# Optimization experiments

Hardware: AMD Instinct MI355X
Metric: run time of the kernel (lower is better)

The kernel has to match this reference:

```python
import jax, jax.numpy as jnp
import numpy as np

B, T, D, H, DK, DV = 2, 2048, 1024, 16, 64, 64
_MASK_ADDER = -10000.0  # tf-models MaskedSoftmax convention


def setup_inputs() -> dict:
    key = jax.random.key(0)
    ks = jax.random.split(key, 8)
    s = 0.02
    return {
        "query": jax.random.normal(ks[0], (B, T, D), jnp.float32),
        "value": jax.random.normal(ks[1], (B, T, D), jnp.float32),
        "Wq": jax.random.normal(ks[2], (D, H, DK), jnp.float32) * s,
        "bq": jnp.zeros((H, DK), jnp.float32),
        "Wk": jax.random.normal(ks[3], (D, H, DK), jnp.float32) * s,
        "bk": jnp.zeros((H, DK), jnp.float32),
        "Wv": jax.random.normal(ks[4], (D, H, DV), jnp.float32) * s,
        "bv": jnp.zeros((H, DV), jnp.float32),
        "Wo": jax.random.normal(ks[5], (H, DV, D), jnp.float32) * s,
        "bo": jnp.zeros((D,), jnp.float32),
        "attention_mask": jnp.ones((B, T, T), jnp.int32),
    }


def reference(query, value, Wq, bq, Wk, bk, Wv, bv, Wo, bo, attention_mask):
    # key defaults to value (call() with key=None); training=False -> no dropout
    q = jnp.einsum("btd,dhk->bthk", query, Wq) + bq          # [B,T,H,DK]
    k = jnp.einsum("bsd,dhk->bshk", value, Wk) + bk          # [B,S,H,DK]
    v = jnp.einsum("bsd,dhk->bshk", value, Wv) + bv          # [B,S,H,DV]
    q = q * (1.0 / jnp.sqrt(jnp.asarray(DK, q.dtype)))
    scores = jnp.einsum("bthk,bshk->bhts", q, k)             # [B,H,T,S]
    # MaskedSoftmax: expand mask at axis 1, additive -10000 on masked slots
    adder = (1.0 - attention_mask.astype(scores.dtype))[:, None, :, :] * _MASK_ADDER
    probs = jax.nn.softmax(scores + adder, axis=-1)
    ctx = jnp.einsum("bhts,bshv->bthv", probs, v)            # [B,T,H,DV]
    out = jnp.einsum("bthv,hvd->btd", ctx, Wo) + bo          # [B,T,D]
    return out
```

## Files before the change

kernel.cpp:

```cpp
#include <hip/hip_runtime.h>
#include <hip/hip_bf16.h>
#include <stdint.h>

#define TSEQ 2048
#define DMODEL 1024
#define NHEAD 16
#define HDIM 64
#define MROWS 4096
#define L2E 1.44269504088896340736f

typedef unsigned short u16;
typedef unsigned int u32;
typedef __attribute__((ext_vector_type(8))) short bf16x8;
typedef __attribute__((ext_vector_type(8))) unsigned short u16x8;
typedef __attribute__((ext_vector_type(4))) unsigned short u16x4;
typedef __attribute__((ext_vector_type(4))) float f32x4;
typedef __attribute__((ext_vector_type(16))) float f32x16;
typedef __attribute__((ext_vector_type(4))) unsigned int u32x4;

__device__ inline u16 f2bf(float f) {
  __hip_bfloat16 h(f);
  return __builtin_bit_cast(u16, h);
}

__device__ inline float fexp2(float x) { float r; asm("v_exp_f32 %0, %1" : "=v"(r) : "v"(x)); return r; }

__device__ inline unsigned cvtpk_bf16(float a, float b) {
  unsigned r; asm("v_cvt_pk_bf16_f32 %0, %1, %2" : "=v"(r) : "v"(a), "v"(b)); return r;
}

__device__ inline void permswap(u32& a, u32& b) {
  asm volatile("v_permlane32_swap_b32 %0, %1" : "+v"(a), "+v"(b));
}

__device__ inline void gload16(const void* g, void* l) {
  __builtin_amdgcn_global_load_lds((const __attribute__((address_space(1))) void*)g,
                                   (__attribute__((address_space(3))) void*)l, 16, 0, 0);
}

__global__ void cvt2(const float* __restrict__ q, const float* __restrict__ v,
                     u16* __restrict__ qo, u16* __restrict__ vo) {
  const float* in = blockIdx.y ? v : q;
  u16* out = blockIdx.y ? vo : qo;
  int i = (blockIdx.x * blockDim.x + threadIdx.x) * 4;
  float4 x = *(const float4*)(in + i);
  u16x4 o;
  o.x = f2bf(x.x); o.y = f2bf(x.y); o.z = f2bf(x.z); o.w = f2bf(x.w);
  *(u16x4*)(out + i) = o;
}

__global__ void wtrans4(const float* __restrict__ Wq, const float* __restrict__ Wk,
                        const float* __restrict__ Wv, const float* __restrict__ Wo,
                        u16* __restrict__ WT3, u16* __restrict__ WoT) {
  __shared__ float tile[32][33];
  const int z = blockIdx.z;
  const float* W = z == 0 ? Wq : z == 1 ? Wk : z == 2 ? Wv : Wo;
  u16* WT = z < 3 ? (WT3 + (size_t)z * 1024 * 1024) : WoT;
  const int bx = blockIdx.x, by = blockIdx.y;
  const int tr = threadIdx.x >> 3;
  const int tc4 = (threadIdx.x & 7) * 4;
  float4 v = *(const float4*)(W + (size_t)(by * 32 + tr) * 1024 + bx * 32 + tc4);
  tile[tr][tc4 + 0] = v.x; tile[tr][tc4 + 1] = v.y;
  tile[tr][tc4 + 2] = v.z; tile[tr][tc4 + 3] = v.w;
  __syncthreads();
  u16x4 o;
  o.x = f2bf(tile[tc4 + 0][tr]); o.y = f2bf(tile[tc4 + 1][tr]);
  o.z = f2bf(tile[tc4 + 2][tr]); o.w = f2bf(tile[tc4 + 3][tr]);
  *(u16x4*)(WT + (size_t)(bx * 32 + tr) * 1024 + by * 32 + tc4) = o;
}

__global__ void maskflag(const int* __restrict__ mask, int* __restrict__ flags) {
  const int st = blockIdx.x, qt = blockIdx.y, b = blockIdx.z;
  const int row = qt * 128 + (threadIdx.x >> 1);
  const int col0 = st * 128 + (threadIdx.x & 1) * 64;
  const int* p = mask + (size_t)b * TSEQ * TSEQ + (size_t)row * TSEQ + col0;
  int ok = 1;
  #pragma unroll
  for (int j = 0; j < 64; j += 4) {
    int4 v = *(const int4*)(p + j);
    ok &= (v.x == 1) & (v.y == 1) & (v.z == 1) & (v.w == 1);
  }
  ok = __all(ok);
  __shared__ int s[4];
  if ((threadIdx.x & 63) == 0) s[threadIdx.x >> 6] = ok;
  __syncthreads();
  if (threadIdx.x == 0) flags[(b * 16 + qt) * 16 + st] = s[0] & s[1] & s[2] & s[3];
}

__global__ void vtrans(const u16* __restrict__ V, u16* __restrict__ VT) {
  __shared__ u16 tile[64][72];
  const int bh = blockIdx.y;
  const int t0 = blockIdx.x * 64;
  const u16* src = V + ((size_t)bh * TSEQ + t0) * 64;
  const int r = threadIdx.x >> 3, sg = threadIdx.x & 7;
  #pragma unroll
  for (int i = 0; i < 2; ++i) {
    int row = r + i * 32;
    u16x8 v = *(const u16x8*)(src + (size_t)row * 64 + sg * 8);
    #pragma unroll
    for (int j = 0; j < 8; ++j) tile[row][sg * 8 + j] = v[j];
  }
  __syncthreads();
  u16* dst = VT + (size_t)bh * 64 * TSEQ;
  #pragma unroll
  for (int i = 0; i < 2; ++i) {
    int v = r + i * 32;
    u16x8 o;
    #pragma unroll
    for (int j = 0; j < 8; ++j) o[j] = tile[sg * 8 + j][v];
    *(u16x8*)(dst + (size_t)v * TSEQ + t0 + sg * 8) = o;
  }
}

__global__ __launch_bounds__(256) void gemm_qkv(
    const u16* __restrict__ qxb, const u16* __restrict__ vxb, const u16* __restrict__ WT3,
    const float* __restrict__ bq, const float* __restrict__ bk, const float* __restrict__ bv,
    u16* __restrict__ Qb, u16* __restrict__ Kb, u16* __restrict__ Vb, float qscale) {
  __shared__ u16 As[128 * 64];
  __shared__ u16 Bs[128 * 64];
  const int tid = threadIdx.x;
  const int w = tid >> 6, lane = tid & 63;
  const int lo = lane & 15, hi = lane >> 4;
  const int m0 = blockIdx.x * 128, n0 = blockIdx.y * 128;
  const int nsel = n0 >> 10;
  const u16* A = nsel == 0 ? qxb : vxb;
  const float* bias = nsel == 0 ? bq : nsel == 1 ? bk : bv;
  u16* dst = nsel == 0 ? Qb : nsel == 1 ? Kb : Vb;
  const float scl = nsel == 0 ? qscale : 1.0f;
  const int wm = (w >> 1) * 64, wn = (w & 1) * 64;
  f32x4 acc[4][4] = {};
  const int loff = w * 4096 + lane * 16;
  for (int kt = 0; kt < 16; ++kt) {
    #pragma unroll
    for (int i = 0; i < 4; ++i) {
      const int off = loff + i * 1024;
      const int row = off >> 7;
      const int g = ((off >> 4) & 7) ^ (row & 7);
      gload16(A + (size_t)(m0 + row) * 1024 + kt * 64 + g * 8, (char*)As + off);
      gload16(WT3 + (size_t)(n0 + row) * 1024 + kt * 64 + g * 8, (char*)Bs + off);
    }
    __syncthreads();
    #pragma unroll
    for (int kk = 0; kk < 2; ++kk) {
      bf16x8 af[4], bfr[4];
      #pragma unroll
      for (int mi = 0; mi < 4; ++mi) {
        int row = wm + mi * 16 + lo;
        af[mi] = *(const bf16x8*)(As + row * 64 + (((kk * 4 + hi) ^ (row & 7)) << 3));
      }
      #pragma unroll
      for (int ni = 0; ni < 4; ++ni) {
        int row = wn + ni * 16 + lo;
        bfr[ni] = *(const bf16x8*)(Bs + row * 64 + (((kk * 4 + hi) ^ (row & 7)) << 3));
      }
      #pragma unroll
      for (int mi = 0; mi < 4; ++mi)
        #pragma unroll
        for (int ni = 0; ni < 4; ++ni)
          acc[mi][ni] = __builtin_amdgcn_mfma_f32_16x16x32_bf16(af[mi], bfr[ni], acc[mi][ni], 0, 0, 0);
    }
    __syncthreads();
  }
  #pragma unroll
  for (int ni = 0; ni < 4; ++ni) {
    const int col = (n0 + wn + ni * 16 + lo) & 1023;
    const float bc = bias[col];
    #pragma unroll
    for (int mi = 0; mi < 4; ++mi) {
      #pragma unroll
      for (int r = 0; r < 4; ++r) {
        const int row = m0 + wm + mi * 16 + hi * 4 + r;
        const float v = (acc[mi][ni][r] + bc) * scl;
        dst[(size_t)(((row >> 11) * NHEAD + (col >> 6)) * TSEQ + (row & 2047)) * HDIM + (col & 63)] = f2bf(v);
      }
    }
  }
}

__global__ __launch_bounds__(256) void gemm_o(const u16* __restrict__ A, const u16* __restrict__ BT,
                                              const float* __restrict__ bias, float* __restrict__ C) {
  __shared__ u16 As[64 * 64];
  __shared__ u16 Bs[128 * 64];
  const int tid = threadIdx.x;
  const int w = tid >> 6, lane = tid & 63;
  const int lo = lane & 15, hi = lane >> 4;
  const int m0 = blockIdx.x * 64, n0 = blockIdx.y * 128;
  const int wm = (w >> 1) * 32, wn = (w & 1) * 64;
  f32x4 acc[2][4] = {};
  for (int kt = 0; kt < 16; ++kt) {
    #pragma unroll
    for (int i = 0; i < 2; ++i) {
      const int off = tid * 16 + i * 4096;
      const int row = off >> 7;
      const int g = ((off >> 4) & 7) ^ (row & 7);
      gload16(A + (size_t)(m0 + row) * 1024 + kt * 64 + g * 8, (char*)As + off);
    }
    #pragma unroll
    for (int i = 0; i < 4; ++i) {
      const int off = tid * 16 + i * 4096;
      const int row = off >> 7;
      const int g = ((off >> 4) & 7) ^ (row & 7);
      gload16(BT + (size_t)(n0 + row) * 1024 + kt * 64 + g * 8, (char*)Bs + off);
    }
    __syncthreads();
    #pragma unroll
    for (int kk = 0; kk < 2; ++kk) {
      bf16x8 af[2], bfr[4];
      #pragma unroll
      for (int mi = 0; mi < 2; ++mi) {
        int row = wm + mi * 16 + lo;
        af[mi] = *(const bf16x8*)(As + row * 64 + (((kk * 4 + hi) ^ (row & 7)) << 3));
      }
      #pragma unroll
      for (int ni = 0; ni < 4; ++ni) {
        int row = wn + ni * 16 + lo;
        bfr[ni] = *(const bf16x8*)(Bs + row * 64 + (((kk * 4 + hi) ^ (row & 7)) << 3));
      }
      #pragma unroll
      for (int mi = 0; mi < 2; ++mi)
        #pragma unroll
        for (int ni = 0; ni < 4; ++ni)
          acc[mi][ni] = __builtin_amdgcn_mfma_f32_16x16x32_bf16(af[mi], bfr[ni], acc[mi][ni], 0, 0, 0);
    }
    __syncthreads();
  }
  #pragma unroll
  for (int ni = 0; ni < 4; ++ni) {
    const int col = n0 + wn + ni * 16 + lo;
    const float bc = bias[col];
    #pragma unroll
    for (int mi = 0; mi < 2; ++mi)
      #pragma unroll
      for (int r = 0; r < 4; ++r) {
        const int row = m0 + wm + mi * 16 + hi * 4 + r;
        C[(size_t)row * DMODEL + col] = acc[mi][ni][r] + bc;
      }
  }
}

__global__ __launch_bounds__(256) void flash(
    const u16* __restrict__ Q, const u16* __restrict__ K, const u16* __restrict__ VT,
    const int* __restrict__ mask, const int* __restrict__ flags, u16* __restrict__ ctx) {
  __shared__ u16 Ks[2][64 * 64];
  __shared__ u16 Vs[3][64 * 64];
  const int tid = threadIdx.x, w = tid >> 6, lane = tid & 63;
  const int l5 = lane & 31, hi2 = lane >> 5;
  const int qt = blockIdx.x, bh = blockIdx.y;
  const int b = bh >> 4, h = bh & 15;
  const int tq = qt * 128 + w * 32;

  const int soff = w * 2048 + lane * 16;
  const int srow0 = w * 16 + (lane >> 3);
  const int lg0 = (((lane & 7) ^ (lane >> 3) ^ ((w * 2) & 3)) << 3);
  const int lg1 = (((lane & 7) ^ (lane >> 3) ^ ((w * 2 + 1) & 3)) << 3);

  bf16x8 qf[4];
  #pragma unroll
  for (int kc = 0; kc < 4; ++kc)
    qf[kc] = *(const bf16x8*)(Q + ((size_t)bh * TSEQ + tq + l5) * 64 + kc * 16 + hi2 * 8);

  unsigned fl = 0;
  {
    const int* fp = flags + (b * 16 + qt) * 16;
    #pragma unroll
    for (int i = 0; i < 4; ++i) {
      int4 v = *(const int4*)(fp + i * 4);
      fl |= (unsigned)((v.x & 1) | ((v.y & 1) << 1) | ((v.z & 1) << 2) | ((v.w & 1) << 3)) << (4 * i);
    }
  }

  f32x16 o0 = {}, o1 = {};
  float mrow = -1e30f, lrow = 0.f;
  bf16x8 paA[4], paB[4];

#define STAGE_K(buf, st_) do {                                                        \
    const u16* kb_ = K + ((size_t)bh * TSEQ + (st_) * 64) * 64;                       \
    gload16(kb_ + (size_t)srow0 * 64 + lg0, (char*)Ks[buf] + soff);                   \
    gload16(kb_ + (size_t)(srow0 + 8) * 64 + lg1, (char*)Ks[buf] + soff + 1024);      \
  } while (0)
#define STAGE_V(buf, st_) do {                                                        \
    const u16* vb_ = VT + (size_t)bh * 64 * TSEQ + (st_) * 64;                        \
    gload16(vb_ + (size_t)srow0 * TSEQ + lg0, (char*)Vs[buf] + soff);                 \
    gload16(vb_ + (size_t)(srow0 + 8) * TSEQ + lg1, (char*)Vs[buf] + soff + 1024);    \
  } while (0)

#define FR(base, row, sg) \
  (*(const bf16x8*)((base) + (row) * 64 + ((((sg) ^ ((row) & 7) ^ (((row) >> 3) & 3)) << 3))))

#define QKC(T, S0, S1) do {                                                           \
    const u16* Kb_ = Ks[(T) & 1];                                                     \
    _Pragma("unroll") for (int kc = 0; kc < 4; ++kc) {                                \
      const int sg = kc * 2 + hi2;                                                    \
      S0 = __builtin_amdgcn_mfma_f32_32x32x16_bf16(FR(Kb_, l5, sg), qf[kc], S0, 0, 0, 0); \
      S1 = __builtin_amdgcn_mfma_f32_32x32x16_bf16(FR(Kb_, 32 + l5, sg), qf[kc], S1, 0, 0, 0); \
    } } while (0)

#define PVC(VB, PA) do {                                                              \
    const u16* Vb_ = Vs[VB];                                                          \
    _Pragma("unroll") for (int kc = 0; kc < 4; ++kc) {                                \
      const int sg = kc * 2 + hi2;                                                    \
      o0 = __builtin_amdgcn_mfma_f32_32x32x16_bf16(PA[kc], FR(Vb_, l5, sg), o0, 0, 0, 0); \
      o1 = __builtin_amdgcn_mfma_f32_32x32x16_bf16(PA[kc], FR(Vb_, 32 + l5, sg), o1, 0, 0, 0); \
    } } while (0)

#define SMAX(T, S0, S1, PAOUT) do {                                                   \
    if (!((fl >> ((T) >> 1)) & 1)) {                                                  \
      const int t_ = tq + l5;                                                         \
      const int* mp_ = mask + ((size_t)b * TSEQ + t_) * TSEQ + (T) * 64;              \
      _Pragma("unroll") for (int r = 0; r < 16; ++r) {                                \
        const int sr_ = (r & 3) + 8 * (r >> 2) + 4 * hi2;                             \
        S0[r] += (1.0f - (float)mp_[sr_]) * -14426.950408f;                           \
        S1[r] += (1.0f - (float)mp_[sr_ + 32]) * -14426.950408f;                      \
      } }                                                                             \
    float c0 = fmaxf(S0[0], S1[0]), c1 = fmaxf(S0[1], S1[1]);                         \
    float c2 = fmaxf(S0[2], S1[2]), c3 = fmaxf(S0[3], S1[3]);                         \
    _Pragma("unroll") for (int r = 4; r < 16; r += 4) {                               \
      c0 = fmaxf(c0, fmaxf(S0[r], S1[r]));     c1 = fmaxf(c1, fmaxf(S0[r+1], S1[r+1])); \
      c2 = fmaxf(c2, fmaxf(S0[r+2], S1[r+2])); c3 = fmaxf(c3, fmaxf(S0[r+3], S1[r+3])); } \
    float pm = fmaxf(fmaxf(c0, c1), fmaxf(c2, c3));                                   \
    pm = fmaxf(pm, __shfl_xor(pm, 32));                                               \
    if (__any(pm - mrow > 11.0f)) {                                                   \
      const float mn_ = fmaxf(mrow, pm);                                              \
      const float a_ = fexp2(mrow - mn_);                                             \
      lrow *= a_; mrow = mn_;                                                         \
      _Pragma("unroll") for (int r = 0; r < 16; ++r) {                                \
        const float ar_ = __shfl(a_, (r & 3) + 8 * (r >> 2) + 4 * hi2);               \
        o0[r] *= ar_; o1[r] *= ar_; } }                                               \
    float rs = 0.f; u32 W0_[8], W1_[8];                                               \
    _Pragma("unroll") for (int q_ = 0; q_ < 4; ++q_)                                  \
      _Pragma("unroll") for (int c_ = 0; c_ < 2; ++c_) {                              \
        const int r = 4 * q_ + 2 * c_;                                                \
        float a0 = fexp2(S0[r] - mrow), b0 = fexp2(S0[r + 1] - mrow);                 \
        float a1 = fexp2(S1[r] - mrow), b1 = fexp2(S1[r + 1] - mrow);                 \
        rs += (a0 + b0) + (a1 + b1);                                                  \
        W0_[q_ * 2 + c_] = cvtpk_bf16(a0, b0);                                        \
        W1_[q_ * 2 + c_] = cvtpk_bf16(a1, b1); }                                      \
    rs += __shfl_xor(rs, 32); lrow += rs;                                             \
    _Pragma("unroll") for (int ts = 0; ts < 2; ++ts)                                  \
      _Pragma("unroll") for (int qp = 0; qp < 2; ++qp) {                              \
        u32 d0 = ts ? W1_[(2 * qp) * 2 + 0] : W0_[(2 * qp) * 2 + 0];                  \
        u32 e0 = ts ? W1_[(2 * qp + 1) * 2 + 0] : W0_[(2 * qp + 1) * 2 + 0];          \
        u32 d1 = ts ? W1_[(2 * qp) * 2 + 1] : W0_[(2 * qp) * 2 + 1];                  \
        u32 e1 = ts ? W1_[(2 * qp + 1) * 2 + 1] : W0_[(2 * qp + 1) * 2 + 1];          \
        permswap(d0, e0); permswap(d1, e1);                                           \
        u32x4 fw_; fw_.x = d0; fw_.y = d1; fw_.z = e0; fw_.w = e1;                    \
        PAOUT[ts * 2 + qp] = __builtin_bit_cast(bf16x8, fw_); }                       \
  } while (0)

#define BODY(T, VPREV, VNEXT, DOSTAGE, PAIN, PAOUT) do {                              \
    if (DOSTAGE) { STAGE_K(((T) + 1) & 1, (T) + 1); STAGE_V(VNEXT, (T) + 1); }        \
    f32x16 s0 = {}, s1 = {};                                                          \
    __builtin_amdgcn_s_setprio(1);                                                    \
    QKC(T, s0, s1);                                                                   \
    PVC(VPREV, PAIN);                                                                 \
    __builtin_amdgcn_s_setprio(0);                                                    \
    SMAX(T, s0, s1, PAOUT);                                                           \
    __syncthreads();                                                                  \
  } while (0)

  STAGE_K(0, 0); STAGE_V(0, 0);
  __syncthreads();
  {
    f32x16 s0 = {}, s1 = {};
    __builtin_amdgcn_s_setprio(1);
    QKC(0, s0, s1);
    __builtin_amdgcn_s_setprio(0);
    STAGE_K(1, 1); STAGE_V(1, 1);
    SMAX(0, s0, s1, paA);
    __syncthreads();
  }

  int vp = 0, vn = 2;
  for (int t = 1; t < 31; t += 2) {
    BODY(t, vp, vn, 1, paA, paB);
    const int vp2 = (vp + 1 == 3) ? 0 : vp + 1;
    const int vn2 = (vn + 1 == 3) ? 0 : vn + 1;
    BODY(t + 1, vp2, vn2, 1, paB, paA);
    vp = (vp2 + 1 == 3) ? 0 : vp2 + 1;
    vn = (vn2 + 1 == 3) ? 0 : vn2 + 1;
  }
  BODY(31, vp, 0, 0, paA, paB);

  __builtin_amdgcn_s_setprio(1);
  PVC(1, paB);
  __builtin_amdgcn_s_setprio(0);

#undef BODY
#undef SMAX
#undef PVC
#undef QKC
#undef FR
#undef STAGE_V
#undef STAGE_K

  const float inv = 1.0f / lrow;
  #pragma unroll
  for (int r = 0; r < 16; ++r) {
    const int sr = (r & 3) + 8 * (r >> 2) + 4 * hi2;
    const float ir = __shfl(inv, sr);
    u16* cp = ctx + (size_t)(b * TSEQ + tq + sr) * DMODEL + h * 64;
    cp[l5] = f2bf(o0[r] * ir);
    cp[32 + l5] = f2bf(o1[r] * ir);
  }
}

extern "C" void kernel_launch(void* const* d_in, const int* in_sizes, int n_in,
                              void* d_out, int out_size, void* d_ws, size_t ws_size,
                              hipStream_t stream) {
  (void)in_sizes; (void)n_in; (void)out_size; (void)ws_size;
  const float* query = (const float*)d_in[0];
  const float* value = (const float*)d_in[1];
  const float* Wq = (const float*)d_in[2];
  const float* bq = (const float*)d_in[3];
  const float* Wk = (const float*)d_in[4];
  const float* bk = (const float*)d_in[5];
  const float* Wv = (const float*)d_in[6];
  const float* bv = (const float*)d_in[7];
  const float* Wo = (const float*)d_in[8];
  const float* bo = (const float*)d_in[9];
  const int* amask = (const int*)d_in[10];

  char* ws = (char*)d_ws;
  const size_t MB = 1 << 20;
  u16* qxb = (u16*)(ws + 0 * MB);
  u16* vxb = (u16*)(ws + 8 * MB);
  u16* WT3 = (u16*)(ws + 16 * MB);
  u16* WoT = (u16*)(ws + 22 * MB);
  u16* Qb  = (u16*)(ws + 24 * MB);
  u16* Kb  = (u16*)(ws + 32 * MB);
  u16* Vb  = (u16*)(ws + 40 * MB);
  u16* VTb = (u16*)(ws + 48 * MB);
  u16* ctx = (u16*)(ws + 56 * MB);
  int* flg = (int*)(ws + 64 * MB);

  cvt2<<<dim3(4096, 2), 256, 0, stream>>>(query, value, qxb, vxb);
  wtrans4<<<dim3(32, 32, 4), 256, 0, stream>>>(Wq, Wk, Wv, Wo, WT3, WoT);
  maskflag<<<dim3(16, 16, 2), 256, 0, stream>>>(amask, flg);

  gemm_qkv<<<dim3(32, 24), 256, 0, stream>>>(qxb, vxb, WT3, bq, bk, bv, Qb, Kb, Vb, 0.125f * L2E);
  vtrans<<<dim3(32, 32), 256, 0, stream>>>(Vb, VTb);
  flash<<<dim3(16, 32), 256, 0, stream>>>(Qb, Kb, VTb, amask, flg, ctx);
  gemm_o<<<dim3(64, 8), 256, 0, stream>>>(ctx, WoT, bo, (float*)d_out);
}
```

Measured before the change: 144.7 us.

## Merge prep kernels, write V transposed from QKV GEMM, swizzle block order

Combines the fp32-to-bf16 conversion, weight transpose and mask-flag kernels into one launch. The QKV GEMM epilogue now writes V directly in transposed layout, which removes the separate vtrans kernel and its round trip through memory. Block indices in gemm_qkv, gemm_o and flash are remapped into XCD-style groups to improve cache locality. The softmax row max uses v_max3. Together these cut launch overhead and extra traffic, at the cost of strided 8-byte stores in the V epilogue.

```diff
diff --git a/kernel.cpp b/kernel.cpp
--- a/kernel.cpp
+++ b/kernel.cpp
@@ -29,6 +29,10 @@
   unsigned r; asm("v_cvt_pk_bf16_f32 %0, %1, %2" : "=v"(r) : "v"(a), "v"(b)); return r;
 }
 
+__device__ inline float fmax3(float a, float b, float c) {
+  float r; asm("v_max3_f32 %0, %1, %2, %3" : "=v"(r) : "v"(a), "v"(b), "v"(c)); return r;
+}
+
 __device__ inline void permswap(u32& a, u32& b) {
   asm volatile("v_permlane32_swap_b32 %0, %1" : "+v"(a), "+v"(b));
 }
@@ -38,94 +42,73 @@
                                    (__attribute__((address_space(3))) void*)l, 16, 0, 0);
 }
 
-__global__ void cvt2(const float* __restrict__ q, const float* __restrict__ v,
-                     u16* __restrict__ qo, u16* __restrict__ vo) {
-  const float* in = blockIdx.y ? v : q;
-  u16* out = blockIdx.y ? vo : qo;
-  int i = (blockIdx.x * blockDim.x + threadIdx.x) * 4;
-  float4 x = *(const float4*)(in + i);
-  u16x4 o;
-  o.x = f2bf(x.x); o.y = f2bf(x.y); o.z = f2bf(x.z); o.w = f2bf(x.w);
-  *(u16x4*)(out + i) = o;
-}
-
-__global__ void wtrans4(const float* __restrict__ Wq, const float* __restrict__ Wk,
-                        const float* __restrict__ Wv, const float* __restrict__ Wo,
-                        u16* __restrict__ WT3, u16* __restrict__ WoT) {
+__global__ void prep(const float* __restrict__ q, const float* __restrict__ v,
+                     u16* __restrict__ qo, u16* __restrict__ vo,
+                     const float* __restrict__ Wq, const float* __restrict__ Wk,
+                     const float* __restrict__ Wv, const float* __restrict__ Wo,
+                     u16* __restrict__ WT3, u16* __restrict__ WoT,
+                     const int* __restrict__ mask, int* __restrict__ flags) {
   __shared__ float tile[32][33];
-  const int z = blockIdx.z;
-  const float* W = z == 0 ? Wq : z == 1 ? Wk : z == 2 ? Wv : Wo;
-  u16* WT = z < 3 ? (WT3 + (size_t)z * 1024 * 1024) : WoT;
-  const int bx = blockIdx.x, by = blockIdx.y;
-  const int tr = threadIdx.x >> 3;
-  const int tc4 = (threadIdx.x & 7) * 4;
-  float4 v = *(const float4*)(W + (size_t)(by * 32 + tr) * 1024 + bx * 32 + tc4);
-  tile[tr][tc4 + 0] = v.x; tile[tr][tc4 + 1] = v.y;
-  tile[tr][tc4 + 2] = v.z; tile[tr][tc4 + 3] = v.w;
-  __syncthreads();
-  u16x4 o;
-  o.x = f2bf(tile[tc4 + 0][tr]); o.y = f2bf(tile[tc4 + 1][tr]);
-  o.z = f2bf(tile[tc4 + 2][tr]); o.w = f2bf(tile[tc4 + 3][tr]);
-  *(u16x4*)(WT + (size_t)(bx * 32 + tr) * 1024 + by * 32 + tc4) = o;
-}
-
-__global__ void maskflag(const int* __restrict__ mask, int* __restrict__ flags) {
-  const int st = blockIdx.x, qt = blockIdx.y, b = blockIdx.z;
-  const int row = qt * 128 + (threadIdx.x >> 1);
-  const int col0 = st * 128 + (threadIdx.x & 1) * 64;
-  const int* p = mask + (size_t)b * TSEQ * TSEQ + (size_t)row * TSEQ + col0;
-  int ok = 1;
-  #pragma unroll
-  for (int j = 0; j < 64; j += 4) {
-    int4 v = *(const int4*)(p + j);
-    ok &= (v.x == 1) & (v.y == 1) & (v.z == 1) & (v.w == 1);
-  }
-  ok = __all(ok);
-  __shared__ int s[4];
-  if ((threadIdx.x & 63) == 0) s[threadIdx.x >> 6] = ok;
-  __syncthreads();
-  if (threadIdx.x == 0) flags[(b * 16 + qt) * 16 + st] = s[0] & s[1] & s[2] & s[3];
-}
-
-__global__ void vtrans(const u16* __restrict__ V, u16* __restrict__ VT) {
-  __shared__ u16 tile[64][72];
-  const int bh = blockIdx.y;
-  const int t0 = blockIdx.x * 64;
-  const u16* src = V + ((size_t)bh * TSEQ + t0) * 64;
-  const int r = threadIdx.x >> 3, sg = threadIdx.x & 7;
-  #pragma unroll
-  for (int i = 0; i < 2; ++i) {
-    int row = r + i * 32;
-    u16x8 v = *(const u16x8*)(src + (size_t)row * 64 + sg * 8);
-    #pragma unroll
-    for (int j = 0; j < 8; ++j) tile[row][sg * 8 + j] = v[j];
-  }
-  __syncthreads();
-  u16* dst = VT + (size_t)bh * 64 * TSEQ;
-  #pragma unroll
-  for (int i = 0; i < 2; ++i) {
-    int v = r + i * 32;
-    u16x8 o;
-    #pragma unroll
-    for (int j = 0; j < 8; ++j) o[j] = tile[sg * 8 + j][v];
-    *(u16x8*)(dst + (size_t)v * TSEQ + t0 + sg * 8) = o;
+  __shared__ int sred[4];
+  const int bid = blockIdx.x, tid = threadIdx.x;
+  if (bid < 8192) {
+    const float* in = bid < 4096 ? q : v;
+    u16* out = bid < 4096 ? qo : vo;
+    const int i = (bid & 4095) * 1024 + tid * 4;
+    float4 x = *(const float4*)(in + i);
+    u16x4 o;
+    o.x = f2bf(x.x); o.y = f2bf(x.y); o.z = f2bf(x.z); o.w = f2bf(x.w);
+    *(u16x4*)(out + i) = o;
+  } else if (bid < 12288) {
+    int t = bid - 8192;
+    const int z = t >> 10; t &= 1023;
+    const float* W = z == 0 ? Wq : z == 1 ? Wk : z == 2 ? Wv : Wo;
+    u16* WT = z < 3 ? (WT3 + (size_t)z * 1024 * 1024) : WoT;
+    const int bx = t & 31, by = t >> 5;
+    const int tr = tid >> 3;
+    const int tc4 = (tid & 7) * 4;
+    float4 x = *(const float4*)(W + (size_t)(by * 32 + tr) * 1024 + bx * 32 + tc4);
+    tile[tr][tc4 + 0] = x.x; tile[tr][tc4 + 1] = x.y;
+    tile[tr][tc4 + 2] = x.z; tile[tr][tc4 + 3] = x.w;
+    __syncthreads();
+    u16x4 o;
+    o.x = f2bf(tile[tc4 + 0][tr]); o.y = f2bf(tile[tc4 + 1][tr]);
+    o.z = f2bf(tile[tc4 + 2][tr]); o.w = f2bf(tile[tc4 + 3][tr]);
+    *(u16x4*)(WT + (size_t)(bx * 32 + tr) * 1024 + by * 32 + tc4) = o;
+  } else {
+    const int t = bid - 12288;
+    const int st = t & 15, qt = (t >> 4) & 15, b = t >> 8;
+    const int row = qt * 128 + (tid >> 1);
+    const int col0 = st * 128 + (tid & 1) * 64;
+    const int* p = mask + (size_t)b * TSEQ * TSEQ + (size_t)row * TSEQ + col0;
+    int ok = 1;
+    #pragma unroll
+    for (int j = 0; j < 64; j += 4) {
+      int4 x = *(const int4*)(p + j);
+      ok &= (x.x == 1) & (x.y == 1) & (x.z == 1) & (x.w == 1);
+    }
+    ok = __all(ok);
+    if ((tid & 63) == 0) sred[tid >> 6] = ok;
+    __syncthreads();
+    if (tid == 0) flags[(b * 16 + qt) * 16 + st] = sred[0] & sred[1] & sred[2] & sred[3];
   }
 }
 
 __global__ __launch_bounds__(256) void gemm_qkv(
     const u16* __restrict__ qxb, const u16* __restrict__ vxb, const u16* __restrict__ WT3,
     const float* __restrict__ bq, const float* __restrict__ bk, const float* __restrict__ bv,
-    u16* __restrict__ Qb, u16* __restrict__ Kb, u16* __restrict__ Vb, float qscale) {
+    u16* __restrict__ Qb, u16* __restrict__ Kb, u16* __restrict__ VTb, float qscale) {
   __shared__ u16 As[128 * 64];
   __shared__ u16 Bs[128 * 64];
   const int tid = threadIdx.x;
   const int w = tid >> 6, lane = tid & 63;
   const int lo = lane & 15, hi = lane >> 4;
-  const int m0 = blockIdx.x * 128, n0 = blockIdx.y * 128;
+  const int bid = blockIdx.x + (blockIdx.y << 5);
+  const int swz = (bid & 7) * 96 + (bid >> 3);
+  const int m0 = (swz & 31) << 7, n0 = (swz >> 5) << 7;
   const int nsel = n0 >> 10;
   const u16* A = nsel == 0 ? qxb : vxb;
   const float* bias = nsel == 0 ? bq : nsel == 1 ? bk : bv;
-  u16* dst = nsel == 0 ? Qb : nsel == 1 ? Kb : Vb;
   const float scl = nsel == 0 ? qscale : 1.0f;
   const int wm = (w >> 1) * 64, wn = (w & 1) * 64;
   f32x4 acc[4][4] = {};
@@ -161,17 +144,36 @@
     }
     __syncthreads();
   }
-  #pragma unroll
-  for (int ni = 0; ni < 4; ++ni) {
-    const int col = (n0 + wn + ni * 16 + lo) & 1023;
-    const float bc = bias[col];
-    #pragma unroll
-    for (int mi = 0; mi < 4; ++mi) {
-      #pragma unroll
-      for (int r = 0; r < 4; ++r) {
-        const int row = m0 + wm + mi * 16 + hi * 4 + r;
-        const float v = (acc[mi][ni][r] + bc) * scl;
-        dst[(size_t)(((row >> 11) * NHEAD + (col >> 6)) * TSEQ + (row & 2047)) * HDIM + (col & 63)] = f2bf(v);
+  if (nsel < 2) {
+    u16* dst = nsel == 0 ? Qb : Kb;
+    #pragma unroll
+    for (int ni = 0; ni < 4; ++ni) {
+      const int col = (n0 + wn + ni * 16 + lo) & 1023;
+      const float bc = bias[col];
+      #pragma unroll
+      for (int mi = 0; mi < 4; ++mi) {
+        #pragma unroll
+        for (int r = 0; r < 4; ++r) {
+          const int row = m0 + wm + mi * 16 + hi * 4 + r;
+          const float v = (acc[mi][ni][r] + bc) * scl;
+          dst[(size_t)(((row >> 11) * NHEAD + (col >> 6)) * TSEQ + (row & 2047)) * HDIM + (col & 63)] = f2bf(v);
+        }
+      }
+    }
+  } else {
+    #pragma unroll
+    for (int ni = 0; ni < 4; ++ni) {
+      const int col = (n0 + wn + ni * 16 + lo) & 1023;
+      const float bc = bias[col];
+      const int v = col & 63;
+      #pragma unroll
+      for (int mi = 0; mi < 4; ++mi) {
+        const int rowb = m0 + wm + mi * 16 + hi * 4;
+        const int bh2 = (rowb >> 11) * NHEAD + (col >> 6);
+        u16x4 pk;
+        #pragma unroll
+        for (int r = 0; r < 4; ++r) pk[r] = f2bf(acc[mi][ni][r] + bc);
+        *(u16x4*)(VTb + ((size_t)bh2 * 64 + v) * TSEQ + (rowb & 2047)) = pk;
       }
     }
   }
@@ -184,7 +186,9 @@
   const int tid = threadIdx.x;
   const int w = tid >> 6, lane = tid & 63;
   const int lo = lane & 15, hi = lane >> 4;
-  const int m0 = blockIdx.x * 64, n0 = blockIdx.y * 128;
+  const int bid = blockIdx.x + (blockIdx.y << 6);
+  const int swz = (bid & 7) * 64 + (bid >> 3);
+  const int m0 = (swz & 63) << 6, n0 = (swz >> 6) << 7;
   const int wm = (w >> 1) * 32, wn = (w & 1) * 64;
   f32x4 acc[2][4] = {};
   for (int kt = 0; kt < 16; ++kt) {
@@ -245,7 +249,9 @@
   __shared__ u16 Vs[3][64 * 64];
   const int tid = threadIdx.x, w = tid >> 6, lane = tid & 63;
   const int l5 = lane & 31, hi2 = lane >> 5;
-  const int qt = blockIdx.x, bh = blockIdx.y;
+  const int bid0 = blockIdx.x + (blockIdx.y << 4);
+  const int swz = (bid0 & 7) * 64 + (bid0 >> 3);
+  const int qt = swz & 15, bh = swz >> 4;
   const int b = bh >> 4, h = bh & 15;
   const int tq = qt * 128 + w * 32;
 
@@ -315,9 +321,9 @@
     float c0 = fmaxf(S0[0], S1[0]), c1 = fmaxf(S0[1], S1[1]);                         \
     float c2 = fmaxf(S0[2], S1[2]), c3 = fmaxf(S0[3], S1[3]);                         \
     _Pragma("unroll") for (int r = 4; r < 16; r += 4) {                               \
-      c0 = fmaxf(c0, fmaxf(S0[r], S1[r]));     c1 = fmaxf(c1, fmaxf(S0[r+1], S1[r+1])); \
-      c2 = fmaxf(c2, fmaxf(S0[r+2], S1[r+2])); c3 = fmaxf(c3, fmaxf(S0[r+3], S1[r+3])); } \
-    float pm = fmaxf(fmaxf(c0, c1), fmaxf(c2, c3));                                   \
+      c0 = fmax3(c0, S0[r], S1[r]);     c1 = fmax3(c1, S0[r+1], S1[r+1]);             \
+      c2 = fmax3(c2, S0[r+2], S1[r+2]); c3 = fmax3(c3, S0[r+3], S1[r+3]); }           \
+    float pm = fmax3(fmaxf(c0, c1), c2, c3);                                          \
     pm = fmaxf(pm, __shfl_xor(pm, 32));                                               \
     if (__any(pm - mrow > 11.0f)) {                                                   \
       const float mn_ = fmaxf(mrow, pm);                                              \
@@ -428,17 +434,12 @@
   u16* WoT = (u16*)(ws + 22 * MB);
   u16* Qb  = (u16*)(ws + 24 * MB);
   u16* Kb  = (u16*)(ws + 32 * MB);
-  u16* Vb  = (u16*)(ws + 40 * MB);
   u16* VTb = (u16*)(ws + 48 * MB);
   u16* ctx = (u16*)(ws + 56 * MB);
   int* flg = (int*)(ws + 64 * MB);
 
-  cvt2<<<dim3(4096, 2), 256, 0, stream>>>(query, value, qxb, vxb);
-  wtrans4<<<dim3(32, 32, 4), 256, 0, stream>>>(Wq, Wk, Wv, Wo, WT3, WoT);
-  maskflag<<<dim3(16, 16, 2), 256, 0, stream>>>(amask, flg);
-
-  gemm_qkv<<<dim3(32, 24), 256, 0, stream>>>(qxb, vxb, WT3, bq, bk, bv, Qb, Kb, Vb, 0.125f * L2E);
-  vtrans<<<dim3(32, 32), 256, 0, stream>>>(Vb, VTb);
+  prep<<<12800, 256, 0, stream>>>(query, value, qxb, vxb, Wq, Wk, Wv, Wo, WT3, WoT, amask, flg);
+  gemm_qkv<<<dim3(32, 24), 256, 0, stream>>>(qxb, vxb, WT3, bq, bk, bv, Qb, Kb, VTb, 0.125f * L2E);
   flash<<<dim3(16, 32), 256, 0, stream>>>(Qb, Kb, VTb, amask, flg, ctx);
   gemm_o<<<dim3(64, 8), 256, 0, stream>>>(ctx, WoT, bo, (float*)d_out);
 }
```

Result: no change. 144.0 us (-0.5%).
